# Kernel optimization log

Hardware: AMD Instinct MI355X
Metric: run time of the kernel (lower is better)

The kernel has to match this reference:

```python
import jax, jax.numpy as jnp
import numpy as np

N_COARSE = 40962   # ico level-6 vertex count
N_NEW = 122880     # level-7 minus level-6 vertices
C_IN = 256
C_OUT = 256


def setup_inputs() -> dict:
    key = jax.random.key(0)
    k1, k2, k3, k4 = jax.random.split(key, 4)
    x = jax.random.normal(k1, (N_COARSE, C_IN), dtype=jnp.float32)
    unpooling_index = jax.random.randint(k2, (N_NEW, 2), 0, N_COARSE, dtype=jnp.int64)
    # nn.Linear params: weight [out, in], bias [out]
    W = jax.random.normal(k3, (C_OUT, C_IN), dtype=jnp.float32) * (1.0 / np.sqrt(C_IN))
    b = jax.random.normal(k4, (C_OUT,), dtype=jnp.float32) * 0.01
    return {"x": x, "unpooling_index": unpooling_index, "W": W, "b": b}


def reference(x, unpooling_index, W, b):
    # Gather the two parent vertices of each new vertex and average them.
    x_up = (x[unpooling_index[:, 0]] + x[unpooling_index[:, 1]]) * 0.5  # [N_NEW, C_IN]
    x_full = jnp.concatenate([x, x_up], axis=0)                          # [N_COARSE+N_NEW, C_IN]
    # nn.Linear: y = x @ W^T + b
    return x_full @ W.T + b
```

## Files before the change

### kernel.cpp

```cpp
#include <hip/hip_runtime.h>
#include <hip/hip_bf16.h>

#define N_COARSE 40962
#define N_NEW    122880
#define M_TOTAL  163842
#define CIN      256
#define COUT     256

#define BK    32
#define NSTEP (CIN / BK)
#define BM    64
#define MT    ((M_TOTAL + BM - 1) / BM)

#define XB_BYTES ((size_t)N_COARSE * CIN * 2)
#define WB_OFF   ((XB_BYTES + 255) & ~(size_t)255)
#define WB_BYTES ((size_t)COUT * CIN * 2)
#define WS_NEED  (WB_OFF + WB_BYTES)

#define XCH   (N_COARSE * CIN / 8)
#define WCH   (COUT * CIN / 8)
#define CVT_T (XCH + WCH)

typedef __bf16 bf16x8 __attribute__((ext_vector_type(8)));
typedef float  f32x4  __attribute__((ext_vector_type(4)));

static __device__ __forceinline__ unsigned short f2bf(float f) {
    unsigned int u = __builtin_bit_cast(unsigned int, f);
    u += 0x7FFFu + ((u >> 16) & 1u);
    return (unsigned short)(u >> 16);
}

#define GLOAD16(gp, lp)                                                        \
    __builtin_amdgcn_global_load_lds(                                          \
        (const __attribute__((address_space(1))) unsigned int*)(gp),           \
        (__attribute__((address_space(3))) unsigned int*)(lp), 16, 0, 0)

__global__ __launch_bounds__(256) void conv_kernel(
    const float* __restrict__ x, const float* __restrict__ W,
    unsigned short* __restrict__ xb, unsigned short* __restrict__ wb)
{
    const int k = blockIdx.x * 256 + threadIdx.x;
    if (k >= CVT_T) return;
    const float* src;
    unsigned short* dst;
    int off;
    if (k < XCH) { src = x; dst = xb; off = k * 8; }
    else         { src = W; dst = wb; off = (k - XCH) * 8; }
    float4 v0 = *(const float4*)(src + off);
    float4 v1 = *(const float4*)(src + off + 4);
    union { unsigned short h[8]; int4 v; } p;
    p.h[0] = f2bf(v0.x); p.h[1] = f2bf(v0.y); p.h[2] = f2bf(v0.z); p.h[3] = f2bf(v0.w);
    p.h[4] = f2bf(v1.x); p.h[5] = f2bf(v1.y); p.h[6] = f2bf(v1.z); p.h[7] = f2bf(v1.w);
    *(int4*)(dst + off) = p.v;
}

__global__ __launch_bounds__(512, 4) void fused_gemm_kernel(
    const unsigned short* __restrict__ xb,
    const int*   __restrict__ idx,
    const unsigned short* __restrict__ wb,
    const float* __restrict__ bias,
    float*       __restrict__ out)
{
    __shared__ __align__(16) unsigned short As[BM * CIN];
    __shared__ __align__(16) unsigned short Ws[2][COUT * BK];

    const int brow = blockIdx.x * BM;
    const int t    = threadIdx.x;
    const int lane = t & 63;
    const int wid  = t >> 6;
    const int wrr  = wid >> 2;
    const int wcc  = wid & 3;
    const char* wbc = (const char*)wb;

#pragma unroll
    for (int i = 0; i < 2; ++i) {
        const int o = wid * 2048 + i * 1024 + lane * 16;
        const int r = o >> 6, c = o & 63;
        GLOAD16(wbc + r * 512 + (c ^ (((r >> 1) & 3) << 4)), (char*)Ws[0] + o);
    }

    {
        const int r  = t >> 3;
        const int q  = t & 7;
        const int gr = brow + r;
        char* arow = (char*)As + r * 512;
        const int swz = (r & 7) << 4;
        const int cb0 = q * 64;
        if (gr < N_COARSE || gr >= M_TOTAL) {
            const int sr = (gr < N_COARSE) ? gr : 0;
            const char* s = (const char*)xb + (size_t)sr * 512 + cb0;
#pragma unroll
            for (int c = 0; c < 4; ++c)
                *(int4*)(arow + ((cb0 + c * 16) ^ swz)) = *(const int4*)(s + c * 16);
        } else {
            const int j  = gr - N_COARSE;
            const int p0 = idx[2 * j];
            const int p1 = idx[2 * j + 1];
            const char* s0 = (const char*)xb + (size_t)p0 * 512 + cb0;
            const char* s1 = (const char*)xb + (size_t)p1 * 512 + cb0;
#pragma unroll
            for (int c = 0; c < 4; ++c) {
                int4 a = *(const int4*)(s0 + c * 16);
                int4 b = *(const int4*)(s1 + c * 16);
                const unsigned int* au = (const unsigned int*)&a;
                const unsigned int* bu = (const unsigned int*)&b;
                union { unsigned short h[8]; int4 v; } p;
#pragma unroll
                for (int e = 0; e < 4; ++e) {
                    const float alo = __builtin_bit_cast(float, au[e] << 16);
                    const float ahi = __builtin_bit_cast(float, au[e] & 0xFFFF0000u);
                    const float blo = __builtin_bit_cast(float, bu[e] << 16);
                    const float bhi = __builtin_bit_cast(float, bu[e] & 0xFFFF0000u);
                    p.h[2 * e]     = f2bf((alo + blo) * 0.5f);
                    p.h[2 * e + 1] = f2bf((ahi + bhi) * 0.5f);
                }
                *(int4*)(arow + ((cb0 + c * 16) ^ swz)) = p.v;
            }
        }
    }

    f32x4 acc[4][2];
#pragma unroll
    for (int j = 0; j < 4; ++j)
#pragma unroll
        for (int i = 0; i < 2; ++i)
            acc[j][i] = (f32x4){0.f, 0.f, 0.f, 0.f};

    __syncthreads();

    for (int ks = 0; ks < NSTEP; ++ks) {
        const int cur = ks & 1;
        if (ks + 1 < NSTEP) {
#pragma unroll
            for (int i = 0; i < 2; ++i) {
                const int o = wid * 2048 + i * 1024 + lane * 16;
                const int r = o >> 6, c = o & 63;
                GLOAD16(wbc + r * 512 + (ks + 1) * 64 + (c ^ (((r >> 1) & 3) << 4)),
                        (char*)Ws[cur ^ 1] + o);
            }
        }

        bf16x8 af[2], wf[4];
        const int acb = ks * 64 + ((lane >> 4) << 4);
#pragma unroll
        for (int i = 0; i < 2; ++i) {
            const int ar = wrr * 32 + i * 16 + (lane & 15);
            af[i] = __builtin_bit_cast(bf16x8,
                *(const int4*)((const char*)As + ar * 512 + (acb ^ ((ar & 7) << 4))));
        }
        const int wcb = (lane >> 4) << 4;
#pragma unroll
        for (int jj = 0; jj < 4; ++jj) {
            const int wr_ = wcc * 64 + jj * 16 + (lane & 15);
            wf[jj] = __builtin_bit_cast(bf16x8,
                *(const int4*)((const char*)Ws[cur] + wr_ * 64 + (wcb ^ (((wr_ >> 1) & 3) << 4))));
        }

#pragma unroll
        for (int jj = 0; jj < 4; ++jj)
#pragma unroll
            for (int i = 0; i < 2; ++i)
                acc[jj][i] = __builtin_amdgcn_mfma_f32_16x16x32_bf16(
                    wf[jj], af[i], acc[jj][i], 0, 0, 0);

        __syncthreads();
    }

    const int nb = wcc * 64 + ((lane >> 4) << 2);
#pragma unroll
    for (int j = 0; j < 4; ++j) {
        const f32x4 bv = __builtin_bit_cast(f32x4, *(const float4*)(bias + nb + j * 16));
#pragma unroll
        for (int i = 0; i < 2; ++i)
            acc[j][i] = acc[j][i] + bv;
    }

    float* Af = (float*)As;
    for (int h = 0; h < 2; ++h) {
        __syncthreads();
        if (wrr == h) {
#pragma unroll
            for (int j = 0; j < 4; ++j)
#pragma unroll
                for (int i = 0; i < 2; ++i) {
                    const int r  = i * 16 + (lane & 15);
                    const int cb = wcc * 256 + j * 64 + ((lane >> 4) << 4);
                    *(f32x4*)((char*)Af + r * 1024 + (cb ^ ((r & 7) << 4))) = acc[j][i];
                }
        }
        __syncthreads();
#pragma unroll
        for (int ri = 0; ri < 4; ++ri) {
            const int r = wid * 4 + ri;
            const f32x4 v = *(const f32x4*)((const char*)Af + r * 1024 +
                                            ((lane * 16) ^ ((r & 7) << 4)));
            const int gr = brow + h * 32 + r;
            if (gr < M_TOTAL)
                *(f32x4*)((char*)out + (size_t)gr * 1024 + lane * 16) = v;
        }
    }
}

union Pk8 { unsigned short h[8]; int4 v; };

__global__ __launch_bounds__(256, 2) void unpool_linear_fused(
    const float* __restrict__ x, const int* __restrict__ idx,
    const float* __restrict__ W, const float* __restrict__ bias,
    float* __restrict__ out)
{
    __shared__ __align__(16) unsigned short As[128 * 64];
    __shared__ __align__(16) unsigned short Bs[128 * 64];
    const int m0 = blockIdx.x * 128;
    const int n0 = blockIdx.y * 128;
    const int t = threadIdx.x, lane = t & 63, wid = t >> 6;
    const int wr = wid >> 1, wc = wid & 1;
    f32x4 acc[4][4];
#pragma unroll
    for (int i = 0; i < 4; ++i)
#pragma unroll
        for (int j = 0; j < 4; ++j) acc[i][j] = (f32x4){0.f,0.f,0.f,0.f};
    for (int k0 = 0; k0 < CIN; k0 += 64) {
#pragma unroll
        for (int i = 0; i < 4; ++i) {
            const int chunk = t + i * 256, r = chunk >> 3, c8 = chunk & 7;
            const int kcol = k0 + c8 * 8;
            const int sidx = (r * 64 + c8 * 8) ^ ((r & 7) << 3);
            float v[8];
            const int gr = m0 + r;
            if (gr < N_COARSE) {
                const float* src = x + (size_t)gr * CIN + kcol;
                float4 a0 = *(const float4*)(src), a1 = *(const float4*)(src + 4);
                v[0]=a0.x; v[1]=a0.y; v[2]=a0.z; v[3]=a0.w;
                v[4]=a1.x; v[5]=a1.y; v[6]=a1.z; v[7]=a1.w;
            } else if (gr < M_TOTAL) {
                const int j = gr - N_COARSE;
                const int p0 = idx[2*j], p1 = idx[2*j+1];
                const float* s0 = x + (size_t)p0 * CIN + kcol;
                const float* s1 = x + (size_t)p1 * CIN + kcol;
                float4 a0=*(const float4*)(s0), a1=*(const float4*)(s0+4);
                float4 b0=*(const float4*)(s1), b1=*(const float4*)(s1+4);
                v[0]=(a0.x+b0.x)*.5f; v[1]=(a0.y+b0.y)*.5f; v[2]=(a0.z+b0.z)*.5f; v[3]=(a0.w+b0.w)*.5f;
                v[4]=(a1.x+b1.x)*.5f; v[5]=(a1.y+b1.y)*.5f; v[6]=(a1.z+b1.z)*.5f; v[7]=(a1.w+b1.w)*.5f;
            } else {
#pragma unroll
                for (int q = 0; q < 8; ++q) v[q] = 0.f;
            }
            Pk8 pa;
#pragma unroll
            for (int q = 0; q < 8; ++q) pa.h[q] = f2bf(v[q]);
            *(int4*)&As[sidx] = pa.v;
            const float* ws = W + (size_t)(n0 + r) * CIN + kcol;
            float4 w0 = *(const float4*)(ws), w1 = *(const float4*)(ws + 4);
            Pk8 pb;
            pb.h[0]=f2bf(w0.x); pb.h[1]=f2bf(w0.y); pb.h[2]=f2bf(w0.z); pb.h[3]=f2bf(w0.w);
            pb.h[4]=f2bf(w1.x); pb.h[5]=f2bf(w1.y); pb.h[6]=f2bf(w1.z); pb.h[7]=f2bf(w1.w);
            *(int4*)&Bs[sidx] = pb.v;
        }
        __syncthreads();
#pragma unroll
        for (int kk = 0; kk < 64; kk += 32) {
            const int kcol = kk + 8 * (lane >> 4);
            bf16x8 af[4], bfv[4];
#pragma unroll
            for (int i = 0; i < 4; ++i) {
                const int r = wr * 64 + i * 16 + (lane & 15);
                af[i] = __builtin_bit_cast(bf16x8, *(const int4*)&As[(r*64+kcol) ^ ((r&7)<<3)]);
            }
#pragma unroll
            for (int j = 0; j < 4; ++j) {
                const int r = wc * 64 + j * 16 + (lane & 15);
                bfv[j] = __builtin_bit_cast(bf16x8, *(const int4*)&Bs[(r*64+kcol) ^ ((r&7)<<3)]);
            }
#pragma unroll
            for (int i = 0; i < 4; ++i)
#pragma unroll
                for (int j = 0; j < 4; ++j)
                    acc[i][j] = __builtin_amdgcn_mfma_f32_16x16x32_bf16(af[i], bfv[j], acc[i][j], 0, 0, 0);
        }
        __syncthreads();
    }
    const int colbase = n0 + wc * 64 + (lane & 15);
    const int rowbase = m0 + wr * 64 + ((lane >> 4) << 2);
#pragma unroll
    for (int j = 0; j < 4; ++j) {
        const int col = colbase + j * 16;
        const float bv = bias[col];
#pragma unroll
        for (int i = 0; i < 4; ++i) {
            const int row = rowbase + i * 16;
#pragma unroll
            for (int r2 = 0; r2 < 4; ++r2) {
                const int rr = row + r2;
                if (rr < M_TOTAL) out[(size_t)rr * COUT + col] = acc[i][j][r2] + bv;
            }
        }
    }
}

extern "C" void kernel_launch(void* const* d_in, const int* in_sizes, int n_in,
                              void* d_out, int out_size, void* d_ws, size_t ws_size,
                              hipStream_t stream) {
    const float* x    = (const float*)d_in[0];
    const int*   idx  = (const int*)d_in[1];
    const float* W    = (const float*)d_in[2];
    const float* bias = (const float*)d_in[3];
    float* out = (float*)d_out;

    if (ws_size >= WS_NEED) {
        unsigned short* xb = (unsigned short*)d_ws;
        unsigned short* wb = (unsigned short*)((char*)d_ws + WB_OFF);
        conv_kernel<<<(CVT_T + 255) / 256, 256, 0, stream>>>(x, W, xb, wb);
        fused_gemm_kernel<<<MT, 512, 0, stream>>>(xb, idx, wb, bias, out);
    } else {
        dim3 grid((M_TOTAL + 127) / 128, COUT / 128);
        unpool_linear_fused<<<grid, 256, 0, stream>>>(x, idx, W, bias, out);
    }
}
```

Before: 76.28 us.

## Prepack W into MFMA fragment order and read B operands directly from global

The conversion kernel now writes bf16 weights in per-lane MFMA fragment order, so each lane reads its B fragment with one contiguous 16-byte global load. This removes the double-buffered LDS staging of W along with the per-k-step __syncthreads. The change frees 32KB of LDS and raises the launch-bounds occupancy hint from 4 to 6. In exchange, every block rereads the 128KB weight matrix from L2/global with no LDS reuse, which puts load latency directly on the MFMA loop.

```diff
diff --git a/kernel.cpp b/kernel.cpp
--- a/kernel.cpp
+++ b/kernel.cpp
@@ -7,8 +7,6 @@
 #define CIN      256
 #define COUT     256
 
-#define BK    32
-#define NSTEP (CIN / BK)
 #define BM    64
 #define MT    ((M_TOTAL + BM - 1) / BM)
 
@@ -30,39 +28,44 @@
     return (unsigned short)(u >> 16);
 }
 
-#define GLOAD16(gp, lp)                                                        \
-    __builtin_amdgcn_global_load_lds(                                          \
-        (const __attribute__((address_space(1))) unsigned int*)(gp),           \
-        (__attribute__((address_space(3))) unsigned int*)(lp), 16, 0, 0)
-
 __global__ __launch_bounds__(256) void conv_kernel(
     const float* __restrict__ x, const float* __restrict__ W,
-    unsigned short* __restrict__ xb, unsigned short* __restrict__ wb)
+    unsigned short* __restrict__ xb, unsigned short* __restrict__ wb2)
 {
     const int k = blockIdx.x * 256 + threadIdx.x;
     if (k >= CVT_T) return;
     const float* src;
     unsigned short* dst;
-    int off;
-    if (k < XCH) { src = x; dst = xb; off = k * 8; }
-    else         { src = W; dst = wb; off = (k - XCH) * 8; }
-    float4 v0 = *(const float4*)(src + off);
-    float4 v1 = *(const float4*)(src + off + 4);
+    if (k < XCH) {
+        src = x + (size_t)k * 8;
+        dst = xb + (size_t)k * 8;
+    } else {
+        const int o  = k - XCH;
+        const int l  = o & 63;
+        const int ks = (o >> 6) & 7;
+        const int f  = (o >> 9) & 3;
+        const int q  = (o >> 11) & 3;
+        const int row = q * 64 + f * 16 + (l & 15);
+        const int ke  = ks * 32 + ((l >> 4) << 3);
+        src = W + (size_t)row * CIN + ke;
+        dst = wb2 + (size_t)o * 8;
+    }
+    float4 v0 = *(const float4*)(src);
+    float4 v1 = *(const float4*)(src + 4);
     union { unsigned short h[8]; int4 v; } p;
     p.h[0] = f2bf(v0.x); p.h[1] = f2bf(v0.y); p.h[2] = f2bf(v0.z); p.h[3] = f2bf(v0.w);
     p.h[4] = f2bf(v1.x); p.h[5] = f2bf(v1.y); p.h[6] = f2bf(v1.z); p.h[7] = f2bf(v1.w);
-    *(int4*)(dst + off) = p.v;
-}
-
-__global__ __launch_bounds__(512, 4) void fused_gemm_kernel(
+    *(int4*)dst = p.v;
+}
+
+__global__ __launch_bounds__(512, 6) void fused_gemm_kernel(
     const unsigned short* __restrict__ xb,
     const int*   __restrict__ idx,
-    const unsigned short* __restrict__ wb,
+    const unsigned short* __restrict__ wb2,
     const float* __restrict__ bias,
     float*       __restrict__ out)
 {
     __shared__ __align__(16) unsigned short As[BM * CIN];
-    __shared__ __align__(16) unsigned short Ws[2][COUT * BK];
 
     const int brow = blockIdx.x * BM;
     const int t    = threadIdx.x;
@@ -70,14 +73,6 @@
     const int wid  = t >> 6;
     const int wrr  = wid >> 2;
     const int wcc  = wid & 3;
-    const char* wbc = (const char*)wb;
-
-#pragma unroll
-    for (int i = 0; i < 2; ++i) {
-        const int o = wid * 2048 + i * 1024 + lane * 16;
-        const int r = o >> 6, c = o & 63;
-        GLOAD16(wbc + r * 512 + (c ^ (((r >> 1) & 3) << 4)), (char*)Ws[0] + o);
-    }
 
     {
         const int r  = t >> 3;
@@ -128,18 +123,10 @@
 
     __syncthreads();
 
-    for (int ks = 0; ks < NSTEP; ++ks) {
-        const int cur = ks & 1;
-        if (ks + 1 < NSTEP) {
-#pragma unroll
-            for (int i = 0; i < 2; ++i) {
-                const int o = wid * 2048 + i * 1024 + lane * 16;
-                const int r = o >> 6, c = o & 63;
-                GLOAD16(wbc + r * 512 + (ks + 1) * 64 + (c ^ (((r >> 1) & 3) << 4)),
-                        (char*)Ws[cur ^ 1] + o);
-            }
-        }
-
+    const char* wbase = (const char*)wb2 + wcc * 32768 + lane * 16;
+
+#pragma unroll
+    for (int ks = 0; ks < 8; ++ks) {
         bf16x8 af[2], wf[4];
         const int acb = ks * 64 + ((lane >> 4) << 4);
 #pragma unroll
@@ -148,22 +135,17 @@
             af[i] = __builtin_bit_cast(bf16x8,
                 *(const int4*)((const char*)As + ar * 512 + (acb ^ ((ar & 7) << 4))));
         }
-        const int wcb = (lane >> 4) << 4;
+#pragma unroll
+        for (int jj = 0; jj < 4; ++jj)
+            wf[jj] = *(const bf16x8*)(wbase + jj * 8192 + ks * 1024);
+
 #pragma unroll
         for (int jj = 0; jj < 4; ++jj) {
-            const int wr_ = wcc * 64 + jj * 16 + (lane & 15);
-            wf[jj] = __builtin_bit_cast(bf16x8,
-                *(const int4*)((const char*)Ws[cur] + wr_ * 64 + (wcb ^ (((wr_ >> 1) & 3) << 4))));
-        }
-
-#pragma unroll
-        for (int jj = 0; jj < 4; ++jj)
-#pragma unroll
-            for (int i = 0; i < 2; ++i)
-                acc[jj][i] = __builtin_amdgcn_mfma_f32_16x16x32_bf16(
-                    wf[jj], af[i], acc[jj][i], 0, 0, 0);
-
-        __syncthreads();
+            acc[jj][0] = __builtin_amdgcn_mfma_f32_16x16x32_bf16(
+                wf[jj], af[0], acc[jj][0], 0, 0, 0);
+            acc[jj][1] = __builtin_amdgcn_mfma_f32_16x16x32_bf16(
+                wf[jj], af[1], acc[jj][1], 0, 0, 0);
+        }
     }
 
     const int nb = wcc * 64 + ((lane >> 4) << 2);
@@ -307,10 +289,10 @@
     float* out = (float*)d_out;
 
     if (ws_size >= WS_NEED) {
-        unsigned short* xb = (unsigned short*)d_ws;
-        unsigned short* wb = (unsigned short*)((char*)d_ws + WB_OFF);
-        conv_kernel<<<(CVT_T + 255) / 256, 256, 0, stream>>>(x, W, xb, wb);
-        fused_gemm_kernel<<<MT, 512, 0, stream>>>(xb, idx, wb, bias, out);
+        unsigned short* xb  = (unsigned short*)d_ws;
+        unsigned short* wb2 = (unsigned short*)((char*)d_ws + WB_OFF);
+        conv_kernel<<<(CVT_T + 255) / 256, 256, 0, stream>>>(x, W, xb, wb2);
+        fused_gemm_kernel<<<MT, 512, 0, stream>>>(xb, idx, wb2, bias, out);
     } else {
         dim3 grid((M_TOTAL + 127) / 128, COUT / 128);
         unpool_linear_fused<<<grid, 256, 0, stream>>>(x, idx, W, bias, out);
```

Result: no change. 75.25 us (-1.4%).
